# Performance work log

Hardware: AMD Instinct MI355X
Metric: run time of the kernel (lower is better)

Reference implementation:

```python
import jax, jax.numpy as jnp
import numpy as np

NUM_CLASSES = 9
BASE_SMOOTHING = 0.1
UPWARD_BIAS = 0.2
BATCH = 4_000_000


def setup_inputs() -> dict:
    key = jax.random.key(0)
    k1, k2 = jax.random.split(key)
    logits = jax.random.normal(k1, (BATCH, NUM_CLASSES), dtype=jnp.float32)
    targets = jax.random.randint(k2, (BATCH,), 0, NUM_CLASSES, dtype=jnp.int32)
    return {"logits": logits, "targets": targets}


def _smooth_labels(targets, num_classes):
    # Closed form of the per-sample Python loop in the torch module:
    #   label[t] = 1 - bs - ub  (set, overwriting the base)
    #   label[k] = bs/C + ub * 0.5**(k - t)   for k > t (geometric halving,
    #              including the last class which keeps remaining*0.5)
    #   label[k] = bs/C                        for k < t
    # followed by row normalization.
    base = BASE_SMOOTHING / num_classes
    main = 1.0 - BASE_SMOOTHING - UPWARD_BIAS
    j = jnp.arange(num_classes)  # [C]
    d = j[None, :] - targets[:, None]  # [B, C], class index minus target
    upward = jnp.where(d > 0, UPWARD_BIAS * jnp.exp2(-d.astype(jnp.float32)), 0.0)
    labels = jnp.where(d == 0, main, base + upward)  # [B, C]
    return labels / labels.sum(axis=-1, keepdims=True)


def reference(logits, targets):
    smooth = _smooth_labels(targets, logits.shape[-1])  # [B, C]
    log_probs = jax.nn.log_softmax(logits, axis=-1)      # [B, C]
    loss = -(smooth * log_probs).sum(axis=-1)            # [B]
    return loss.mean()
```

## Files before the change

### kernel.cpp

```cpp
#include <hip/hip_runtime.h>
#include <math.h>

#define NUM_C 9
constexpr float BASE_SMOOTH = 0.1f;
constexpr float W_BASE = BASE_SMOOTH / (float)NUM_C;
constexpr float W_MAIN = 0.7f;

constexpr int THREADS = 256;
constexpr int ROWS_PER_BLOCK = 1024;
constexpr int FLOATS_PER_BLOCK = ROWS_PER_BLOCK * NUM_C;
constexpr int VEC_PER_THREAD = FLOATS_PER_BLOCK / 4 / THREADS;
constexpr int ROWS_PER_THREAD = ROWS_PER_BLOCK / THREADS;

__global__ __launch_bounds__(THREADS) void ccel_main(
    const float* __restrict__ logits,
    const int* __restrict__ targets,
    float* __restrict__ partials,
    int nRows)
{
    __shared__ float lds[FLOATS_PER_BLOCK];
    __shared__ float wave_sums[THREADS / 64];

    const int tid = threadIdx.x;
    const long long totalVecs = ((long long)nRows * NUM_C) / 4;
    const long long vecBase = (long long)blockIdx.x * (FLOATS_PER_BLOCK / 4);

    const float4* __restrict__ gv = (const float4*)logits;
    float4* ldsv = (float4*)lds;

#pragma unroll
    for (int i = 0; i < VEC_PER_THREAD; i++) {
        long long vi = vecBase + (long long)(i * THREADS + tid);
        if (vi < totalVecs) {
            ldsv[i * THREADS + tid] = gv[vi];
        }
    }
    __syncthreads();

    const int rowBase = blockIdx.x * ROWS_PER_BLOCK;
    float acc = 0.0f;

#pragma unroll
    for (int i = 0; i < ROWS_PER_THREAD; i++) {
        const int lr = tid + i * THREADS;
        const int r = rowBase + lr;
        if (r < nRows) {
            const float* x = &lds[lr * NUM_C];
            const int t = targets[r];

            float m = x[0];
#pragma unroll
            for (int j = 1; j < NUM_C; j++) m = fmaxf(m, x[j]);

            float s = 0.0f;
            float weighted = 0.0f;
#pragma unroll
            for (int j = 0; j < NUM_C; j++) {
                const float xj = x[j];
                s += __expf(xj - m);
                const int d = j - t;
                float w;
                if (d == 0)      w = W_MAIN;
                else if (d > 0)  w = W_BASE + 0.2f * exp2f((float)(-d));
                else             w = W_BASE;
                weighted += w * xj;
            }
            const float lse = m + __logf(s);
            const float S = 0.98888889f - 0.2f * exp2f((float)(t - 8));
            acc += lse - weighted / S;
        }
    }

#pragma unroll
    for (int off = 32; off > 0; off >>= 1)
        acc += __shfl_down(acc, off, 64);

    if ((tid & 63) == 0) wave_sums[tid >> 6] = acc;
    __syncthreads();
    if (tid == 0) {
        float bsum = 0.0f;
#pragma unroll
        for (int w = 0; w < THREADS / 64; w++) bsum += wave_sums[w];
        partials[blockIdx.x] = bsum;
    }
}

__global__ __launch_bounds__(THREADS) void ccel_finish(
    const float* __restrict__ partials,
    int n,
    float* __restrict__ out,
    float invBatch)
{
    double acc = 0.0;
    for (int i = threadIdx.x; i < n; i += THREADS)
        acc += (double)partials[i];

#pragma unroll
    for (int off = 32; off > 0; off >>= 1)
        acc += __shfl_down(acc, off, 64);

    __shared__ double wave_sums[THREADS / 64];
    if ((threadIdx.x & 63) == 0) wave_sums[threadIdx.x >> 6] = acc;
    __syncthreads();
    if (threadIdx.x == 0) {
        double total = 0.0;
#pragma unroll
        for (int w = 0; w < THREADS / 64; w++) total += wave_sums[w];
        out[0] = (float)(total * (double)invBatch);
    }
}

extern "C" void kernel_launch(void* const* d_in, const int* in_sizes, int n_in,
                              void* d_out, int out_size, void* d_ws, size_t ws_size,
                              hipStream_t stream) {
    const float* logits = (const float*)d_in[0];
    const int* targets = (const int*)d_in[1];
    const int nRows = in_sizes[1];

    float* partials = (float*)d_ws;
    const int nBlocks = (nRows + ROWS_PER_BLOCK - 1) / ROWS_PER_BLOCK;

    ccel_main<<<nBlocks, THREADS, 0, stream>>>(logits, targets, partials, nRows);
    ccel_finish<<<1, THREADS, 0, stream>>>(partials, nBlocks, (float*)d_out,
                                           1.0f / (float)nRows);
}
```

Measured before the change: 227.4 us.

## Use async global-to-LDS loads and process four contiguous rows per thread

Full blocks now copy logits into LDS with global_load_lds async copies instead of staging through registers. Each thread handles four consecutive rows: it loads their 36 floats as nine float4 reads from LDS and the four targets as one int4. The weighted sum is rebuilt algebraically from the row sum, the target logit and a halving suffix recurrence, and the division becomes a hardware reciprocal. Contiguous per-thread LDS reads of 36 floats may cause bank conflicts, and the 36-float register array raises register pressure; the finish kernel now uses 1024 threads.

```diff
diff --git a/kernel.cpp b/kernel.cpp
--- a/kernel.cpp
+++ b/kernel.cpp
@@ -2,72 +2,95 @@
 #include <math.h>
 
 #define NUM_C 9
-constexpr float BASE_SMOOTH = 0.1f;
-constexpr float W_BASE = BASE_SMOOTH / (float)NUM_C;
+constexpr float W_BASE = 0.1f / 9.0f;
 constexpr float W_MAIN = 0.7f;
 
 constexpr int THREADS = 256;
 constexpr int ROWS_PER_BLOCK = 1024;
-constexpr int FLOATS_PER_BLOCK = ROWS_PER_BLOCK * NUM_C;
-constexpr int VEC_PER_THREAD = FLOATS_PER_BLOCK / 4 / THREADS;
-constexpr int ROWS_PER_THREAD = ROWS_PER_BLOCK / THREADS;
+constexpr int VECS_PER_BLOCK = ROWS_PER_BLOCK * NUM_C / 4;
+constexpr int VECS_PER_WAVE = VECS_PER_BLOCK / 4;
+constexpr int CALLS_PER_WAVE = VECS_PER_WAVE / 64;
 
-__global__ __launch_bounds__(THREADS) void ccel_main(
+__device__ __forceinline__ void async_copy16(const float4* g, float4* l) {
+    __builtin_amdgcn_global_load_lds(
+        (const __attribute__((address_space(1))) void*)g,
+        (__attribute__((address_space(3))) void*)l,
+        16 , 0 , 0 );
+}
+
+__global__ __launch_bounds__(THREADS, 4) void ccel_main(
     const float* __restrict__ logits,
     const int* __restrict__ targets,
     float* __restrict__ partials,
-    int nRows)
+    int nRows, int nFullBlocks)
 {
-    __shared__ float lds[FLOATS_PER_BLOCK];
+    __shared__ float4 lds4[VECS_PER_BLOCK];
     __shared__ float wave_sums[THREADS / 64];
 
     const int tid = threadIdx.x;
-    const long long totalVecs = ((long long)nRows * NUM_C) / 4;
-    const long long vecBase = (long long)blockIdx.x * (FLOATS_PER_BLOCK / 4);
+    const int wave = tid >> 6;
+    const int lane = tid & 63;
+    const long long vecBase = (long long)blockIdx.x * VECS_PER_BLOCK;
+    const float4* gv = (const float4*)logits + vecBase;
 
-    const float4* __restrict__ gv = (const float4*)logits;
-    float4* ldsv = (float4*)lds;
-
+    if (blockIdx.x < nFullBlocks) {
+        const float4* src = gv + wave * VECS_PER_WAVE;
+        float4* dst = lds4 + wave * VECS_PER_WAVE;
 #pragma unroll
-    for (int i = 0; i < VEC_PER_THREAD; i++) {
-        long long vi = vecBase + (long long)(i * THREADS + tid);
-        if (vi < totalVecs) {
-            ldsv[i * THREADS + tid] = gv[vi];
+        for (int i = 0; i < CALLS_PER_WAVE; i++) {
+            async_copy16(src + i * 64 + lane, dst + i * 64);
+        }
+    } else {
+        const long long totalVecs = ((long long)nRows * NUM_C) / 4;
+        for (int i = tid; i < VECS_PER_BLOCK; i += THREADS) {
+            if (vecBase + i < totalVecs) lds4[i] = gv[i];
         }
     }
     __syncthreads();
 
-    const int rowBase = blockIdx.x * ROWS_PER_BLOCK;
+    const int myRow = blockIdx.x * ROWS_PER_BLOCK + tid * 4;
     float acc = 0.0f;
 
+    if (myRow < nRows) {
+        const int4 t4 = ((const int4*)targets)[myRow >> 2];
+        const int tg[4] = {t4.x, t4.y, t4.z, t4.w};
+
+        float x[36];
+        float4* xv = (float4*)x;
 #pragma unroll
-    for (int i = 0; i < ROWS_PER_THREAD; i++) {
-        const int lr = tid + i * THREADS;
-        const int r = rowBase + lr;
-        if (r < nRows) {
-            const float* x = &lds[lr * NUM_C];
-            const int t = targets[r];
+        for (int i = 0; i < 9; i++) xv[i] = lds4[tid * 9 + i];
 
-            float m = x[0];
 #pragma unroll
-            for (int j = 1; j < NUM_C; j++) m = fmaxf(m, x[j]);
+        for (int k = 0; k < 4; k++) {
+            const float* xr = x + k * NUM_C;
+            const int t = tg[k];
 
-            float s = 0.0f;
-            float weighted = 0.0f;
+            float m = xr[0];
+#pragma unroll
+            for (int j = 1; j < NUM_C; j++) m = fmaxf(m, xr[j]);
+
+            float sum = 0.0f, xt = 0.0f;
 #pragma unroll
             for (int j = 0; j < NUM_C; j++) {
-                const float xj = x[j];
-                s += __expf(xj - m);
-                const int d = j - t;
-                float w;
-                if (d == 0)      w = W_MAIN;
-                else if (d > 0)  w = W_BASE + 0.2f * exp2f((float)(-d));
-                else             w = W_BASE;
-                weighted += w * xj;
+                sum += xr[j];
+                xt = (t == j) ? xr[j] : xt;
             }
-            const float lse = m + __logf(s);
-            const float S = 0.98888889f - 0.2f * exp2f((float)(t - 8));
-            acc += lse - weighted / S;
+
+            float g = 0.0f, gt = 0.0f;
+#pragma unroll
+            for (int j = NUM_C - 1; j >= 1; j--) {
+                g = 0.5f * (xr[j] + g);
+                gt = (t == j - 1) ? g : gt;
+            }
+
+            float es = 0.0f;
+#pragma unroll
+            for (int j = 0; j < NUM_C; j++) es += __expf(xr[j] - m);
+            const float lse = m + __logf(es);
+
+            const float S = 0.98888889f - 0.2f * ldexpf(1.0f, t - 8);
+            const float weighted = W_BASE * sum + (W_MAIN - W_BASE) * xt + 0.2f * gt;
+            acc += lse - weighted * __builtin_amdgcn_rcpf(S);
         }
     }
 
@@ -75,7 +98,7 @@
     for (int off = 32; off > 0; off >>= 1)
         acc += __shfl_down(acc, off, 64);
 
-    if ((tid & 63) == 0) wave_sums[tid >> 6] = acc;
+    if (lane == 0) wave_sums[wave] = acc;
     __syncthreads();
     if (tid == 0) {
         float bsum = 0.0f;
@@ -85,27 +108,27 @@
     }
 }
 
-__global__ __launch_bounds__(THREADS) void ccel_finish(
+__global__ __launch_bounds__(1024) void ccel_finish(
     const float* __restrict__ partials,
     int n,
     float* __restrict__ out,
     float invBatch)
 {
     double acc = 0.0;
-    for (int i = threadIdx.x; i < n; i += THREADS)
+    for (int i = threadIdx.x; i < n; i += 1024)
         acc += (double)partials[i];
 
 #pragma unroll
     for (int off = 32; off > 0; off >>= 1)
         acc += __shfl_down(acc, off, 64);
 
-    __shared__ double wave_sums[THREADS / 64];
-    if ((threadIdx.x & 63) == 0) wave_sums[threadIdx.x >> 6] = acc;
+    __shared__ double wsum[16];
+    if ((threadIdx.x & 63) == 0) wsum[threadIdx.x >> 6] = acc;
     __syncthreads();
     if (threadIdx.x == 0) {
         double total = 0.0;
 #pragma unroll
-        for (int w = 0; w < THREADS / 64; w++) total += wave_sums[w];
+        for (int w = 0; w < 16; w++) total += wsum[w];
         out[0] = (float)(total * (double)invBatch);
     }
 }
@@ -119,8 +142,11 @@
 
     float* partials = (float*)d_ws;
     const int nBlocks = (nRows + ROWS_PER_BLOCK - 1) / ROWS_PER_BLOCK;
+    const long long totalVecs = ((long long)nRows * NUM_C) / 4;
+    const int nFullBlocks = (int)(totalVecs / VECS_PER_BLOCK);
 
-    ccel_main<<<nBlocks, THREADS, 0, stream>>>(logits, targets, partials, nRows);
-    ccel_finish<<<1, THREADS, 0, stream>>>(partials, nBlocks, (float*)d_out,
-                                           1.0f / (float)nRows);
+    ccel_main<<<nBlocks, THREADS, 0, stream>>>(logits, targets, partials,
+                                               nRows, nFullBlocks);
+    ccel_finish<<<1, 1024, 0, stream>>>(partials, nBlocks, (float*)d_out,
+                                        1.0f / (float)nRows);
 }
```

Result: faster. 213.9 us (-5.9%).
